# Performance work log

Hardware: AMD Instinct MI355X
Metric: run time of the kernel (lower is better)

Reference implementation:

```python
import jax, jax.numpy as jnp
import numpy as np

NUM_HEADS = 16
KEY_DIM = 128
VALUE_DIM = 128
HIDDEN = 2048


def setup_inputs() -> dict:
    key = jax.random.key(0)
    k1, k2, k3 = jax.random.split(key, 3)
    B, T = 4, 2048
    hidden_states = jax.random.normal(k1, (B, T, HIDDEN), dtype=jnp.float32)
    # qkv_proj: Linear(hidden, H*(2*key_dim+value_dim)) no bias -> weight (out, in)
    qkv_out = NUM_HEADS * (2 * KEY_DIM + VALUE_DIM)
    w_qkv = jax.random.normal(k2, (qkv_out, HIDDEN), dtype=jnp.float32) * (1.0 / np.sqrt(HIDDEN))
    w_out = jax.random.normal(k3, (HIDDEN, NUM_HEADS * VALUE_DIM), dtype=jnp.float32) * (1.0 / np.sqrt(NUM_HEADS * VALUE_DIM))
    b_out = jnp.zeros((HIDDEN,), dtype=jnp.float32)
    return {"hidden_states": hidden_states, "w_qkv": w_qkv, "w_out": w_out, "b_out": b_out}


def reference(hidden_states, w_qkv, w_out, b_out):
    B, T, _ = hidden_states.shape
    H, Dk, Dv = NUM_HEADS, KEY_DIM, VALUE_DIM
    scale = 1.0 / np.sqrt(Dk).astype(np.float32)
    qkv = hidden_states @ w_qkv.T  # (B,T,H*(2Dk+Dv))
    q, k, v = jnp.split(qkv, [H * Dk, 2 * H * Dk], axis=-1)
    q = q.reshape(B, T, H, Dk).transpose(0, 2, 1, 3)  # (B,H,T,Dk)
    k = k.reshape(B, T, H, Dk).transpose(0, 2, 1, 3)
    v = v.reshape(B, T, H, Dv).transpose(0, 2, 1, 3)
    scores = jnp.einsum('bhtd,bhsd->bhts', q, k) * scale  # (B,H,T,S)
    causal = jnp.tril(jnp.ones((T, T), dtype=bool))
    scores = jnp.where(causal[None, None], scores, jnp.float32(-jnp.inf))
    attn = jax.nn.softmax(scores, axis=-1)
    out = jnp.einsum('bhts,bhsd->bhtd', attn, v)  # (B,H,T,Dv)
    out = out.transpose(0, 2, 1, 3).reshape(B, T, H * Dv)
    return out @ w_out.T + b_out
```

## Files before the change

### kernel.cpp

```cpp
#include <hip/hip_runtime.h>
#include <hip/hip_bf16.h>
#include <stdint.h>

#define HID   2048
#define NH    16
#define QKV_N 6144
#define BT    8192
#define TT    2048

typedef short bf16x8  __attribute__((ext_vector_type(8)));
typedef float f32x4   __attribute__((ext_vector_type(4)));
typedef float f32x16  __attribute__((ext_vector_type(16)));
typedef unsigned short u16;

__device__ __forceinline__ u16 f2bf(float f){
  union { float f; unsigned u; } v; v.f = f;
  unsigned r = 0x7fffu + ((v.u >> 16) & 1u);
  return (u16)((v.u + r) >> 16);
}
__device__ __forceinline__ float bf2f(u16 x){
  union { unsigned u; float f; } v; v.u = ((unsigned)x) << 16;
  return v.f;
}
__device__ __forceinline__ unsigned cvt_pk_bf16(float lo, float hi){
  unsigned r;
  asm("v_cvt_pk_bf16_f32 %0, %1, %2" : "=v"(r) : "v"(lo), "v"(hi));
  return r;
}

typedef __attribute__((address_space(3))) void lds_vt;
typedef const __attribute__((address_space(1))) void gbl_vt;

__device__ __forceinline__ void gload16(const void* g, void* l){
  __builtin_amdgcn_global_load_lds((gbl_vt*)g, (lds_vt*)l, 16, 0, 0);
}

#define FENCE() asm volatile("" ::: "memory")
#define SYNC()  { FENCE(); __builtin_amdgcn_s_barrier(); FENCE(); }

__global__ __launch_bounds__(256) void cvt_bf16(const float* __restrict__ in,
                                                u16* __restrict__ out, int n4){
  int i = blockIdx.x * blockDim.x + threadIdx.x;
  int stride = gridDim.x * blockDim.x;
  for (; i < n4; i += stride){
    float4 v = ((const float4*)in)[i];
    ushort4 o;
    o.x = f2bf(v.x); o.y = f2bf(v.y); o.z = f2bf(v.z); o.w = f2bf(v.w);
    ((ushort4*)out)[i] = o;
  }
}

template<int OUT_BF16>
__global__ __launch_bounds__(512, 2) void gemm256(const u16* __restrict__ A,
                                                  const u16* __restrict__ Bm,
                                                  u16* __restrict__ Cb,
                                                  float* __restrict__ Cf,
                                                  const float* __restrict__ bias,
                                                  int M, int N, int K)
{
  __shared__ u16 lds[4 * 256 * 64];
  u16* const Abuf[2] = { lds,          lds + 16384 };
  u16* const Bbuf[2] = { lds + 32768,  lds + 49152 };

  const int tid  = threadIdx.x;
  const int w    = tid >> 6;
  const int lane = tid & 63;
  const int wm   = w >> 2;
  const int wn   = w & 3;
  const int lr   = lane & 15;
  const int lg   = lane >> 4;

  int bid = blockIdx.x;
  { int qq = gridDim.x >> 3; bid = (bid & 7) * qq + (bid >> 3); }
  const int ntile = N >> 8;
  const int m0 = (bid / ntile) << 8;
  const int n0 = (bid % ntile) << 8;

  const int rS = tid >> 3;
  const int cS = ((tid & 7) ^ (rS & 7)) * 8;
  const u16* gA = A  + (size_t)(m0 + rS) * K + cS;
  const u16* gB = Bm + (size_t)(n0 + rS) * K + cS;
  const int wds = w * 512;

  f32x4 acc[8][4] = {};
  bf16x8 aq[2][2], bq[4][2];

  auto stgA = [&](int buf, int half, int kt){
    const u16* s = gA + (size_t)(half * 128) * K + (size_t)kt * 64;
    gload16(s,                  Abuf[buf] + half * 8192 + wds);
    gload16(s + (size_t)64 * K, Abuf[buf] + half * 8192 + 4096 + wds);
  };
  auto stgB = [&](int buf, int half, int kt){
    const u16* s = gB + (size_t)(half * 128) * K + (size_t)kt * 64;
    gload16(s,                  Bbuf[buf] + half * 8192 + wds);
    gload16(s + (size_t)64 * K, Bbuf[buf] + half * 8192 + 4096 + wds);
  };
  auto loadA = [&](const u16* ab, int q){
    #pragma unroll
    for (int kk = 0; kk < 2; ++kk){
      #pragma unroll
      for (int mf2 = 0; mf2 < 2; ++mf2){
        int row = wm * 128 + (q * 2 + mf2) * 16 + lr;
        int blk = (kk * 4 + lg) ^ (lr & 7);
        aq[mf2][kk] = *(const bf16x8*)(ab + row * 64 + blk * 8);
      }
    }
  };
  auto loadB = [&](const u16* bb){
    #pragma unroll
    for (int nf = 0; nf < 4; ++nf){
      #pragma unroll
      for (int kk = 0; kk < 2; ++kk){
        int row = wn * 64 + nf * 16 + lr;
        int blk = (kk * 4 + lg) ^ (lr & 7);
        bq[nf][kk] = *(const bf16x8*)(bb + row * 64 + blk * 8);
      }
    }
  };

#define MFMAQ(Q) do {                                                         \
    __builtin_amdgcn_s_setprio(1);                                            \
    _Pragma("unroll")                                                         \
    for (int kk = 0; kk < 2; ++kk){                                           \
      _Pragma("unroll")                                                       \
      for (int mf2 = 0; mf2 < 2; ++mf2){                                      \
        _Pragma("unroll")                                                     \
        for (int nf = 0; nf < 4; ++nf)                                        \
          acc[(Q)*2+mf2][nf] = __builtin_amdgcn_mfma_f32_16x16x32_bf16(       \
              aq[mf2][kk], bq[nf][kk], acc[(Q)*2+mf2][nf], 0, 0, 0);          \
      }                                                                       \
    }                                                                         \
    __builtin_amdgcn_s_setprio(0);                                            \
  } while (0)

  stgA(0, 0, 0); stgA(0, 1, 0);
  stgB(0, 0, 0); stgB(0, 1, 0);
  stgB(1, 0, 1); stgB(1, 1, 1);
  asm volatile("s_waitcnt vmcnt(4)" ::: "memory");
  SYNC();

  const int NI = K >> 7;
  for (int it = 0; it < NI; ++it){
    const int t = it * 2;
    const bool lastI = (it == NI - 1);

    loadB(Bbuf[0]);
    loadA(Abuf[0], 0);
    stgA(1, 0, t + 1);
    SYNC(); MFMAQ(0); SYNC();

    loadA(Abuf[0], 1);
    stgA(1, 1, t + 1);
    SYNC(); MFMAQ(1); SYNC();

    loadA(Abuf[0], 2);
    if (!lastI) stgB(0, 0, t + 2);
    SYNC(); MFMAQ(2); SYNC();

    loadA(Abuf[0], 3);
    if (!lastI) stgB(0, 1, t + 2);
    SYNC(); MFMAQ(3);
    if (lastI) asm volatile("s_waitcnt vmcnt(0)" ::: "memory");
    else       asm volatile("s_waitcnt vmcnt(4)" ::: "memory");
    SYNC();

    loadB(Bbuf[1]);
    loadA(Abuf[1], 0);
    if (!lastI) stgA(0, 0, t + 2);
    SYNC(); MFMAQ(0); SYNC();

    loadA(Abuf[1], 1);
    if (!lastI) stgA(0, 1, t + 2);
    SYNC(); MFMAQ(1); SYNC();

    loadA(Abuf[1], 2);
    if (!lastI) stgB(1, 0, t + 3);
    SYNC(); MFMAQ(2); SYNC();

    loadA(Abuf[1], 3);
    if (!lastI) stgB(1, 1, t + 3);
    SYNC(); MFMAQ(3);
    if (!lastI) asm volatile("s_waitcnt vmcnt(4)" ::: "memory");
    SYNC();
  }
#undef MFMAQ

  const int orow = m0 + wm * 128 + lg * 4;
  const int ocol = n0 + wn * 64 + lr;
  #pragma unroll
  for (int mf = 0; mf < 8; ++mf)
    #pragma unroll
    for (int nf = 0; nf < 4; ++nf)
      #pragma unroll
      for (int r = 0; r < 4; ++r){
        int row = orow + mf * 16 + r;
        int col = ocol + nf * 16;
        float v = acc[mf][nf][r];
        if (OUT_BF16)
          Cb[(size_t)row * N + col] = f2bf(v);
        else
          Cf[(size_t)row * N + col] = v + bias[col];
      }
}

__global__ __launch_bounds__(256) void vtrans(const u16* __restrict__ qkv,
                                              u16* __restrict__ vt2){
  __shared__ u16 tile[32][136];
  const int t5 = blockIdx.x;
  const int bh = blockIdx.y;
  const int b = bh >> 4, h = bh & 15;
  const int tid = threadIdx.x;

  #pragma unroll
  for (int p = 0; p < 2; ++p){
    int idx = p * 256 + tid;
    int row = idx >> 4;
    int c8  = (idx & 15) * 8;
    bf16x8 v = *(const bf16x8*)(qkv + (size_t)(b * TT + t5 * 32 + row) * QKV_N + 4096 + h * 128 + c8);
    *(bf16x8*)(&tile[row][c8]) = v;
  }
  __syncthreads();
  u16* outp = vt2 + (size_t)(bh * 64 + t5) * 4096;
  #pragma unroll
  for (int p = 0; p < 2; ++p){
    int id = p * 256 + tid;
    int r  = id >> 3;
    int sp = id & 7;
    int sl = sp ^ (r & 7);
    int d  = (sl >> 2) * 64 + r;
    int kv = (sl & 3) * 8;
    bf16x8 v;
    #pragma unroll
    for (int e = 0; e < 8; ++e) v[e] = (short)tile[kv + e][d];
    *(bf16x8*)(outp + id * 8) = v;
  }
}

__global__ __launch_bounds__(256, 4) void attn(const u16* __restrict__ qkv,
                                               const u16* __restrict__ vt2,
                                               u16* __restrict__ aout)
{
  __shared__ u16 Kl[2][32 * 128];
  __shared__ u16 Vl[2][64 * 64];

  const int qt = 15 - (int)blockIdx.y;
  const int bh = blockIdx.x;
  const int b = bh >> 4, h = bh & 15;
  const int tid  = threadIdx.x;
  const int w    = tid >> 6;
  const int lane = tid & 63;
  const int l31  = lane & 31;
  const int hi   = lane >> 5;
  const int sw7  = l31 & 7;

  const int qg = qt * 128 + w * 32 + l31;
  const float sc2 = 0.08838834764831845f * 1.4426950408889634f;

  bf16x8 qf[8];
  {
    const u16* qp = qkv + (size_t)(b * TT + qg) * QKV_N + h * 128 + hi * 8;
    #pragma unroll
    for (int s = 0; s < 8; ++s){
      bf16x8 raw = *(const bf16x8*)(qp + s * 16);
      unsigned pk[4];
      #pragma unroll
      for (int p2 = 0; p2 < 4; ++p2)
        pk[p2] = cvt_pk_bf16(bf2f((u16)raw[2 * p2]) * sc2,
                             bf2f((u16)raw[2 * p2 + 1]) * sc2);
      int4 u = { (int)pk[0], (int)pk[1], (int)pk[2], (int)pk[3] };
      qf[s] = *(bf16x8*)&u;
    }
  }

  f32x16 o[4] = {};
  float lsum = 0.f;

  const u16* ksrc = qkv + (size_t)(b * TT + (tid >> 4)) * QKV_N + 2048 + h * 128
                    + (((tid & 15) ^ ((tid >> 4) & 7)) * 8);
  const u16* vsrc = vt2 + (size_t)bh * (64 * 4096) + tid * 8;

  auto stage = [&](int buf, int j){
    const u16* ks = ksrc + (size_t)(j * 32) * QKV_N;
    gload16(ks,                    &Kl[buf][tid * 8]);
    gload16(ks + (size_t)16 * QKV_N, &Kl[buf][2048 + tid * 8]);
    const u16* vs = vsrc + (size_t)j * 4096;
    gload16(vs,        &Vl[buf][tid * 8]);
    gload16(vs + 2048, &Vl[buf][2048 + tid * 8]);
  };

  const int NT  = 4 * qt + 4;
  const int jme = qt * 4 + w;
  stage(0, 0);

  for (int j = 0; j < NT; ++j){
    const int cur = j & 1;
    SYNC();
    if (j + 1 < NT){
      stage(cur ^ 1, j + 1);
      asm volatile("s_waitcnt vmcnt(4)" ::: "memory");
    } else {
      asm volatile("s_waitcnt vmcnt(0)" ::: "memory");
    }
    SYNC();

    if (j <= jme){
      f32x16 s = {};
      const u16* KB = Kl[cur];
      __builtin_amdgcn_s_setprio(1);
      #pragma unroll
      for (int sl = 0; sl < 8; ++sl){
        const int sp = ((sl * 2 + hi) ^ sw7) * 8;
        bf16x8 kf = *(const bf16x8*)(KB + l31 * 128 + sp);
        s = __builtin_amdgcn_mfma_f32_32x32x16_bf16(kf, qf[sl], s, 0, 0, 0);
      }
      __builtin_amdgcn_s_setprio(0);

      if (j == jme){
        #pragma unroll
        for (int r = 0; r < 16; ++r){
          const int krow = (r & 3) + 8 * (r >> 2) + 4 * hi;
          if (krow > l31) s[r] = -3.0e38f;
        }
      }

      #pragma unroll
      for (int r = 0; r < 16; ++r) s[r] = exp2f(s[r]);
      {
        float t0 = (s[0] + s[1]) + (s[2] + s[3]);
        float t1 = (s[4] + s[5]) + (s[6] + s[7]);
        float t2 = (s[8] + s[9]) + (s[10] + s[11]);
        float t3 = (s[12] + s[13]) + (s[14] + s[15]);
        lsum += (t0 + t1) + (t2 + t3);
      }

      bf16x8 pf[2];
      #pragma unroll
      for (int kb = 0; kb < 2; ++kb){
        const int R0 = kb * 8;
        const unsigned wa0 = cvt_pk_bf16(s[R0],     s[R0 + 1]);
        const unsigned wa1 = cvt_pk_bf16(s[R0 + 2], s[R0 + 3]);
        const unsigned wb0 = cvt_pk_bf16(s[R0 + 4], s[R0 + 5]);
        const unsigned wb1 = cvt_pk_bf16(s[R0 + 6], s[R0 + 7]);
        const int s0 = hi ? (int)wa0 : (int)wb0;
        const int s1 = hi ? (int)wa1 : (int)wb1;
        const int r0 = __shfl_xor(s0, 32, 64);
        const int r1 = __shfl_xor(s1, 32, 64);
        int4 u;
        u.x = hi ? r0 : (int)wa0;
        u.y = hi ? r1 : (int)wa1;
        u.z = hi ? (int)wb0 : r0;
        u.w = hi ? (int)wb1 : r1;
        pf[kb] = *(bf16x8*)&u;
      }

      const u16* VB = Vl[cur];
      __builtin_amdgcn_s_setprio(1);
      #pragma unroll
      for (int db = 0; db < 4; ++db){
        const int r6 = (db & 1) * 32 + l31;
        const int hd = db >> 1;
        #pragma unroll
        for (int kb = 0; kb < 2; ++kb){
          const int sp = ((hd * 4 + kb * 2 + hi) ^ sw7) * 8;
          bf16x8 vf = *(const bf16x8*)(VB + r6 * 64 + sp);
          o[db] = __builtin_amdgcn_mfma_f32_32x32x16_bf16(vf, pf[kb], o[db], 0, 0, 0);
        }
      }
      __builtin_amdgcn_s_setprio(0);
    }
  }

  const float lt = lsum + __shfl_xor(lsum, 32, 64);
  const float inv = 1.0f / lt;
  u16* op = aout + (size_t)(b * TT + qg) * HID + h * 128;
  #pragma unroll
  for (int db = 0; db < 4; ++db)
    #pragma unroll
    for (int rq = 0; rq < 4; ++rq){
      ushort4 pk;
      pk.x = f2bf(o[db][rq * 4 + 0] * inv);
      pk.y = f2bf(o[db][rq * 4 + 1] * inv);
      pk.z = f2bf(o[db][rq * 4 + 2] * inv);
      pk.w = f2bf(o[db][rq * 4 + 3] * inv);
      *(ushort4*)(op + db * 32 + rq * 8 + hi * 4) = pk;
    }
}

extern "C" void kernel_launch(void* const* d_in, const int* in_sizes, int n_in,
                              void* d_out, int out_size, void* d_ws, size_t ws_size,
                              hipStream_t stream)
{
  (void)in_sizes; (void)n_in; (void)out_size; (void)ws_size;
  const float* hs    = (const float*)d_in[0];
  const float* w_qkv = (const float*)d_in[1];
  const float* w_out = (const float*)d_in[2];
  const float* b_out = (const float*)d_in[3];
  float* out = (float*)d_out;

  char* ws = (char*)d_ws;
  u16* qkv_bf  = (u16*)(ws);
  u16* wout_bf = (u16*)(ws + 100663296);
  u16* hs_bf   = (u16*)(ws + 109051904);
  u16* attn_bf = hs_bf;
  u16* wqkv_bf = (u16*)(ws + 142606336);
  u16* vt2_bf  = wqkv_bf;

  cvt_bf16<<<2048, 256, 0, stream>>>(hs,    hs_bf,   (BT * HID) / 4);
  cvt_bf16<<<2048, 256, 0, stream>>>(w_qkv, wqkv_bf, (QKV_N * HID) / 4);
  cvt_bf16<<<1024, 256, 0, stream>>>(w_out, wout_bf, (HID * 2048) / 4);

  gemm256<1><<<(BT / 256) * (QKV_N / 256), 512, 0, stream>>>(
      hs_bf, wqkv_bf, qkv_bf, nullptr, nullptr, BT, QKV_N, HID);

  vtrans<<<dim3(TT / 32, 64), 256, 0, stream>>>(qkv_bf, vt2_bf);

  attn<<<dim3(64, 16), 256, 0, stream>>>(qkv_bf, vt2_bf, attn_bf);

  gemm256<0><<<(BT / 256) * (HID / 256), 512, 0, stream>>>(
      attn_bf, wout_bf, nullptr, out, b_out, BT, HID, HID);
}
```

Baseline: 426.6 us.

## Make GEMMs persistent with cross-tile prefetch and XCD-aware tile mapping

```diff
diff --git a/kernel.cpp b/kernel.cpp
--- a/kernel.cpp
+++ b/kernel.cpp
@@ -70,31 +70,37 @@
   const int lr   = lane & 15;
   const int lg   = lane >> 4;
 
-  int bid = blockIdx.x;
-  { int qq = gridDim.x >> 3; bid = (bid & 7) * qq + (bid >> 3); }
-  const int ntile = N >> 8;
-  const int m0 = (bid / ntile) << 8;
-  const int n0 = (bid % ntile) << 8;
+  const int ntn   = N >> 8;
+  const int chunk = (32 * ntn) >> 3;
+  const int tpb   = chunk >> 5;
+  const int xcd   = blockIdx.x & 7;
+  const int sslot = blockIdx.x >> 3;
 
   const int rS = tid >> 3;
   const int cS = ((tid & 7) ^ (rS & 7)) * 8;
-  const u16* gA = A  + (size_t)(m0 + rS) * K + cS;
-  const u16* gB = Bm + (size_t)(n0 + rS) * K + cS;
   const int wds = w * 512;
 
-  f32x4 acc[8][4] = {};
-  bf16x8 aq[2][2], bq[4][2];
-
-  auto stgA = [&](int buf, int half, int kt){
-    const u16* s = gA + (size_t)(half * 128) * K + (size_t)kt * 64;
+  auto tileMN = [&](int idx, int& tm0, int& tn0){
+    int ml = (idx >> 3) & 3;
+    int nl = (idx & 7) | ((idx >> 5) << 3);
+    tm0 = ((xcd << 2) + ml) << 8;
+    tn0 = nl << 8;
+  };
+
+  auto stgAb = [&](const u16* base, int buf, int half, int kt){
+    const u16* s = base + (size_t)(half * 128) * K + (size_t)kt * 64;
     gload16(s,                  Abuf[buf] + half * 8192 + wds);
     gload16(s + (size_t)64 * K, Abuf[buf] + half * 8192 + 4096 + wds);
   };
-  auto stgB = [&](int buf, int half, int kt){
-    const u16* s = gB + (size_t)(half * 128) * K + (size_t)kt * 64;
+  auto stgBb = [&](const u16* base, int buf, int half, int kt){
+    const u16* s = base + (size_t)(half * 128) * K + (size_t)kt * 64;
     gload16(s,                  Bbuf[buf] + half * 8192 + wds);
     gload16(s + (size_t)64 * K, Bbuf[buf] + half * 8192 + 4096 + wds);
   };
+
+  f32x4 acc[8][4];
+  bf16x8 aq[2][2], bq[4][2];
+
   auto loadA = [&](const u16* ab, int q){
     #pragma unroll
     for (int kk = 0; kk < 2; ++kk){
@@ -133,74 +139,102 @@
     __builtin_amdgcn_s_setprio(0);                                            \
   } while (0)
 
-  stgA(0, 0, 0); stgA(0, 1, 0);
-  stgB(0, 0, 0); stgB(0, 1, 0);
-  stgB(1, 0, 1); stgB(1, 1, 1);
-  asm volatile("s_waitcnt vmcnt(4)" ::: "memory");
-  SYNC();
-
   const int NI = K >> 7;
-  for (int it = 0; it < NI; ++it){
-    const int t = it * 2;
-    const bool lastI = (it == NI - 1);
-
-    loadB(Bbuf[0]);
-    loadA(Abuf[0], 0);
-    stgA(1, 0, t + 1);
-    SYNC(); MFMAQ(0); SYNC();
-
-    loadA(Abuf[0], 1);
-    stgA(1, 1, t + 1);
-    SYNC(); MFMAQ(1); SYNC();
-
-    loadA(Abuf[0], 2);
-    if (!lastI) stgB(0, 0, t + 2);
-    SYNC(); MFMAQ(2); SYNC();
-
-    loadA(Abuf[0], 3);
-    if (!lastI) stgB(0, 1, t + 2);
-    SYNC(); MFMAQ(3);
-    if (lastI) asm volatile("s_waitcnt vmcnt(0)" ::: "memory");
-    else       asm volatile("s_waitcnt vmcnt(4)" ::: "memory");
-    SYNC();
-
-    loadB(Bbuf[1]);
-    loadA(Abuf[1], 0);
-    if (!lastI) stgA(0, 0, t + 2);
-    SYNC(); MFMAQ(0); SYNC();
-
-    loadA(Abuf[1], 1);
-    if (!lastI) stgA(0, 1, t + 2);
-    SYNC(); MFMAQ(1); SYNC();
-
-    loadA(Abuf[1], 2);
-    if (!lastI) stgB(1, 0, t + 3);
-    SYNC(); MFMAQ(2); SYNC();
-
-    loadA(Abuf[1], 3);
-    if (!lastI) stgB(1, 1, t + 3);
-    SYNC(); MFMAQ(3);
-    if (!lastI) asm volatile("s_waitcnt vmcnt(4)" ::: "memory");
-    SYNC();
+  int idx = sslot;
+
+  for (int ti = 0; ti < tpb; ++ti, idx += 32){
+    const bool hasNext = (ti + 1 < tpb);
+    int m0, n0, m0n = 0, n0n = 0;
+    tileMN(idx, m0, n0);
+    if (hasNext) tileMN(idx + 32, m0n, n0n);
+
+    const u16* gA  = A  + (size_t)(m0  + rS) * K + cS;
+    const u16* gB  = Bm + (size_t)(n0  + rS) * K + cS;
+    const u16* gAn = A  + (size_t)(m0n + rS) * K + cS;
+    const u16* gBn = Bm + (size_t)(n0n + rS) * K + cS;
+
+    if (ti == 0){
+      stgAb(gA, 0, 0, 0); stgAb(gA, 0, 1, 0);
+      stgBb(gB, 0, 0, 0); stgBb(gB, 0, 1, 0);
+      stgBb(gB, 1, 0, 1); stgBb(gB, 1, 1, 1);
+      asm volatile("s_waitcnt vmcnt(4)" ::: "memory");
+      SYNC();
+    }
+
+    #pragma unroll
+    for (int mf = 0; mf < 8; ++mf)
+      #pragma unroll
+      for (int nf = 0; nf < 4; ++nf)
+        acc[mf][nf] = (f32x4){0.f, 0.f, 0.f, 0.f};
+
+    for (int it = 0; it < NI; ++it){
+      const int t = it * 2;
+      const bool lastI = (it == NI - 1);
+
+      loadB(Bbuf[0]);
+      loadA(Abuf[0], 0);
+      stgAb(gA, 1, 0, t + 1);
+      SYNC(); MFMAQ(0); SYNC();
+      loadA(Abuf[0], 1);
+      stgAb(gA, 1, 1, t + 1);
+      SYNC(); MFMAQ(1); SYNC();
+      loadA(Abuf[0], 2);
+      if (!lastI)       stgBb(gB,  0, 0, t + 2);
+      else if (hasNext) stgBb(gBn, 0, 0, 0);
+      SYNC(); MFMAQ(2); SYNC();
+      loadA(Abuf[0], 3);
+      if (!lastI)       stgBb(gB,  0, 1, t + 2);
+      else if (hasNext) stgBb(gBn, 0, 1, 0);
+      SYNC(); MFMAQ(3);
+      if (lastI && !hasNext) asm volatile("s_waitcnt vmcnt(0)" ::: "memory");
+      else                   asm volatile("s_waitcnt vmcnt(4)" ::: "memory");
+      SYNC();
+      loadB(Bbuf[1]);
+      loadA(Abuf[1], 0);
+      if (!lastI)       stgAb(gA,  0, 0, t + 2);
+      else if (hasNext) stgAb(gAn, 0, 0, 0);
+      SYNC(); MFMAQ(0); SYNC();
+      loadA(Abuf[1], 1);
+      if (!lastI)       stgAb(gA,  0, 1, t + 2);
+      else if (hasNext) stgAb(gAn, 0, 1, 0);
+      SYNC(); MFMAQ(1); SYNC();
+      loadA(Abuf[1], 2);
+      if (!lastI)       stgBb(gB,  1, 0, t + 3);
+      else if (hasNext) stgBb(gBn, 1, 0, 1);
+      SYNC(); MFMAQ(2); SYNC();
+      loadA(Abuf[1], 3);
+      if (!lastI)       stgBb(gB,  1, 1, t + 3);
+      else if (hasNext) stgBb(gBn, 1, 1, 1);
+      SYNC(); MFMAQ(3);
+      if (!lastI){
+        asm volatile("s_waitcnt vmcnt(4)" ::: "memory");
+        SYNC();
+      }
+    }
+
+    const int orow = m0 + wm * 128 + lg * 4;
+    const int ocol = n0 + wn * 64 + lr;
+    #pragma unroll
+    for (int mf = 0; mf < 8; ++mf)
+      #pragma unroll
+      for (int nf = 0; nf < 4; ++nf)
+        #pragma unroll
+        for (int r = 0; r < 4; ++r){
+          int row = orow + mf * 16 + r;
+          int col = ocol + nf * 16;
+          float v = acc[mf][nf][r];
+          if (OUT_BF16)
+            Cb[(size_t)row * N + col] = f2bf(v);
+          else
+            Cf[(size_t)row * N + col] = v + bias[col];
+        }
+
+    if (hasNext){
+      asm volatile("s_waitcnt vmcnt(4)" ::: "memory");
+      SYNC();
+    }
   }
 #undef MFMAQ
-
-  const int orow = m0 + wm * 128 + lg * 4;
-  const int ocol = n0 + wn * 64 + lr;
-  #pragma unroll
-  for (int mf = 0; mf < 8; ++mf)
-    #pragma unroll
-    for (int nf = 0; nf < 4; ++nf)
-      #pragma unroll
-      for (int r = 0; r < 4; ++r){
-        int row = orow + mf * 16 + r;
-        int col = ocol + nf * 16;
-        float v = acc[mf][nf][r];
-        if (OUT_BF16)
-          Cb[(size_t)row * N + col] = f2bf(v);
-        else
-          Cf[(size_t)row * N + col] = v + bias[col];
-      }
 }
 
 __global__ __launch_bounds__(256) void vtrans(const u16* __restrict__ qkv,
@@ -243,7 +277,9 @@
   __shared__ u16 Kl[2][32 * 128];
   __shared__ u16 Vl[2][64 * 64];
 
-  const int qt = 15 - (int)blockIdx.y;
+  const int y = (int)blockIdx.y;
+  const int qt = (y < 4) ? (15 - y) : (y < 8) ? (y + 4)
+               : (y < 12) ? (y - 4) : (15 - y);
   const int bh = blockIdx.x;
   const int b = bh >> 4, h = bh & 15;
   const int tid  = threadIdx.x;
@@ -281,7 +317,7 @@
 
   auto stage = [&](int buf, int j){
     const u16* ks = ksrc + (size_t)(j * 32) * QKV_N;
-    gload16(ks,                    &Kl[buf][tid * 8]);
+    gload16(ks,                      &Kl[buf][tid * 8]);
     gload16(ks + (size_t)16 * QKV_N, &Kl[buf][2048 + tid * 8]);
     const u16* vs = vsrc + (size_t)j * 4096;
     gload16(vs,        &Vl[buf][tid * 8]);
@@ -409,13 +445,13 @@
   cvt_bf16<<<2048, 256, 0, stream>>>(w_qkv, wqkv_bf, (QKV_N * HID) / 4);
   cvt_bf16<<<1024, 256, 0, stream>>>(w_out, wout_bf, (HID * 2048) / 4);
 
-  gemm256<1><<<(BT / 256) * (QKV_N / 256), 512, 0, stream>>>(
+  gemm256<1><<<256, 512, 0, stream>>>(
       hs_bf, wqkv_bf, qkv_bf, nullptr, nullptr, BT, QKV_N, HID);
 
   vtrans<<<dim3(TT / 32, 64), 256, 0, stream>>>(qkv_bf, vt2_bf);
 
   attn<<<dim3(64, 16), 256, 0, stream>>>(qkv_bf, vt2_bf, attn_bf);
 
-  gemm256<0><<<(BT / 256) * (HID / 256), 512, 0, stream>>>(
+  gemm256<0><<<256, 512, 0, stream>>>(
       attn_bf, wout_bf, nullptr, out, b_out, BT, HID, HID);
 }
```

Result: slower. 446.3 us (+4.6%).
